# Kernel tuning notes

Measured on AMD Instinct MI355X. Metric: run time of the kernel, lower is better.

The kernel has to match this reference:

```python
import jax, jax.numpy as jnp
import numpy as np
from jax import lax

N, L, C_IN, NOISE_C, COMP, NC = 256, 512, 514, 112, 16, 2
MAIN_IN = NOISE_C + COMP  # 128
FEAT = NC * 4 * L         # 4096

def _conv1d(x, w, b, pad):
    # x [N,C,L], w [O,I,K]
    y = lax.conv_general_dilated(x, w, (1,), [(pad, pad)], dimension_numbers=('NCH', 'OIH', 'NCH'))
    return y + b[None, :, None]

def _bn(x, g, b):
    # BatchNorm1d, training mode: biased batch stats over (N, L)
    m = x.mean(axis=(0, 2), keepdims=True)
    v = x.var(axis=(0, 2), keepdims=True)
    return (x - m) * lax.rsqrt(v + 1e-5) * g[None, :, None] + b[None, :, None]

def _lrelu(x):
    return jnp.where(x >= 0, x, 0.2 * x)

def _pos_encode(length, dim):
    j = np.arange(dim)
    div = 1.0 / np.power(10000.0, 2 * (j[:, None] // 2) / dim)   # [dim,1]
    ang = np.arange(length)[None, :] * div                       # [dim,length]
    ang = np.where((j % 2 == 0)[:, None], np.sin(ang), np.cos(ang))
    return jnp.asarray(ang[None], jnp.float32)                   # [1,dim,length]

def _assemble(circle_prob, slider_prob):
    # Vectorized run-length label expansion equivalent to the per-sample python while-loop.
    # circle_prob [N, L/2, 2], slider_prob [N, L/4, 2] -> [N, L, 3]
    n, B = slider_prob.shape[0], slider_prob.shape[1]
    c = jnp.argmax(circle_prob, -1)
    s = jnp.argmax(slider_prob, -1)
    zc = jnp.zeros(circle_prob.shape[:-1] + (1,), circle_prob.dtype)
    zs = jnp.zeros(slider_prob.shape[:-1] + (1,), slider_prob.dtype)
    cp3 = jnp.concatenate([circle_prob, zc], -1)                                   # insert 0 at class 2
    sp3 = jnp.concatenate([slider_prob[..., :1], zs, slider_prob[..., 1:]], -1)    # insert 0 at class 1
    pad100 = jnp.array([1., 0., 0.], cp3.dtype)
    pad001 = jnp.array([0., 0., 1.], cp3.dtype)
    bidx = jnp.arange(B)[None, :]
    # slider-body blocks: slider run continues and not cut by sequence end
    body = (s == 1) & (bidx < B - 1)
    prev_body = jnp.concatenate([jnp.zeros((n, 1), bool), body[:, :-1]], 1)
    # tail block ends a slider run (either run stops, or boundary block)
    tail = ((s == 1) & (bidx == B - 1)) | ((s == 0) & prev_body)
    # circle emission for each half-step: prob row if predicted circle else pad
    cr0 = jnp.where((c == 1)[..., None], cp3, pad100).reshape(n, B, 2, 3)
    bodyE = body[..., None]
    row0 = jnp.where((body | tail)[..., None], sp3, cr0[:, :, 0, :])
    row1 = jnp.where(bodyE, pad001, pad100)
    row2 = jnp.where(bodyE, pad001, cr0[:, :, 1, :])
    row3 = jnp.where(bodyE, pad001, pad100)
    return jnp.stack([row0, row1, row2, row3], 2).reshape(n, 4 * B, 3)

def _forward(noise, cond_data, gumbel_u, ext_w1, ext_b1, ext_w2, ext_b2, ext_bn_g, ext_bn_b,
             m_w1, m_b1, m_w2, m_b2, m_bn_g, m_bn_b, lin_w, lin_b, circ_w, circ_b, slid_w, slid_b):
    # FeatureExtractor
    x = cond_data.transpose(0, 2, 1)                      # [N, 514, L]
    x = _lrelu(_conv1d(x, ext_w1, ext_b1, 0))             # [N, 32, L]
    cond = _bn(_conv1d(x, ext_w2, ext_b2, 1), ext_bn_g, ext_bn_b)  # [N, 16, L]
    gen_in = jnp.concatenate([cond, noise.transpose(0, 2, 1)], 1) + _pos_encode(L, MAIN_IN)  # [N,128,L]
    h = _lrelu(_conv1d(gen_in, m_w1, m_b1, 3))            # [N, 32, L]
    h = _lrelu(_bn(_conv1d(h, m_w2, m_b2, 1), m_bn_g, m_bn_b))     # [N, 8, L]
    flat = _lrelu(h.reshape(h.shape[0], -1) @ lin_w + lin_b)       # [N, 4096]
    circle_prob = (flat @ circ_w + circ_b).reshape(-1, L // 2, NC)
    slider_prob = (flat @ slid_w + slid_b).reshape(-1, L // 4, NC)
    out = _assemble(circle_prob, slider_prob)             # [N, L, 3]
    # gumbel_softmax(hard=True, tau=1)
    g = -jnp.log(-jnp.log(gumbel_u + 1e-10) + 1e-10)
    logits = out + g
    y_soft = jax.nn.softmax(logits, -1)
    y_hard = jax.nn.one_hot(jnp.argmax(logits, -1), 3, dtype=y_soft.dtype)
    gen_out = y_hard + y_soft - lax.stop_gradient(y_soft)
    return gen_out, cond

def setup_inputs() -> dict:
    key = jax.random.key(0)
    ks = jax.random.split(key, 12)
    def rn(k, shape, fan_in):
        return jax.random.normal(k, shape, jnp.float32) * (1.0 / fan_in) ** 0.5
    return {
        'noise': jax.random.normal(ks[0], (N, L, NOISE_C), jnp.float32),
        'cond_data': jax.random.normal(ks[1], (N, L, C_IN), jnp.float32),
        'gumbel_u': jax.random.uniform(ks[2], (N, L, 3), jnp.float32),
        'ext_w1': rn(ks[3], (C_IN // 16, C_IN, 1), C_IN), 'ext_b1': jnp.zeros(C_IN // 16),
        'ext_w2': rn(ks[4], (COMP, C_IN // 16, 3), 3 * (C_IN // 16)), 'ext_b2': jnp.zeros(COMP),
        'ext_bn_g': jnp.ones(COMP), 'ext_bn_b': jnp.zeros(COMP),
        'm_w1': rn(ks[5], (NC * 16, MAIN_IN, 7), 7 * MAIN_IN), 'm_b1': jnp.zeros(NC * 16),
        'm_w2': rn(ks[6], (NC * 4, NC * 16, 3), 3 * NC * 16), 'm_b2': jnp.zeros(NC * 4),
        'm_bn_g': jnp.ones(NC * 4), 'm_bn_b': jnp.zeros(NC * 4),
        'lin_w': rn(ks[7], (FEAT, FEAT), FEAT), 'lin_b': jnp.zeros(FEAT),
        'circ_w': rn(ks[8], (FEAT, NC * L // 2), FEAT), 'circ_b': jnp.zeros(NC * L // 2),
        'slid_w': rn(ks[9], (FEAT, NC * L // 4), FEAT), 'slid_b': jnp.zeros(NC * L // 4),
    }

def reference(noise, cond_data, gumbel_u, ext_w1, ext_b1, ext_w2, ext_b2, ext_bn_g, ext_bn_b,
              m_w1, m_b1, m_w2, m_b2, m_bn_g, m_bn_b, lin_w, lin_b, circ_w, circ_b, slid_w, slid_b):
    return _forward(noise, cond_data, gumbel_u, ext_w1, ext_b1, ext_w2, ext_b2, ext_bn_g, ext_bn_b,
                    m_w1, m_b1, m_w2, m_b2, m_bn_g, m_bn_b, lin_w, lin_b, circ_w, circ_b, slid_w, slid_b)
```

## Files before the change

### kernel.cpp

```cpp
#include <hip/hip_runtime.h>
#include <math.h>

#define NB 256
#define LL 512
#define CIN 514

__device__ __forceinline__ float lrelu(float x) { return x >= 0.f ? x : 0.2f * x; }

__global__ __launch_bounds__(256) void k_pos(float* __restrict__ pos) {
    int idx = blockIdx.x * 256 + threadIdx.x;
    int c = idx >> 9, l = idx & 511;
    double e = (double)(2 * (c >> 1)) / 128.0;
    double dv = 1.0 / pow(10000.0, e);
    double a = (double)l * dv;
    pos[idx] = (float)((c & 1) ? cos(a) : sin(a));
}

__global__ __launch_bounds__(256) void k_posconv(const float* __restrict__ POS, const float* __restrict__ W,
                                                 const float* __restrict__ bias, float* __restrict__ PC) {
    const int t = threadIdx.x;
    const int o = blockIdx.x >> 4, l0 = (blockIdx.x & 15) * 32;
    const int l = l0 + (t & 31), cs = t >> 5;
    float acc = 0.f;
    for (int ci = 0; ci < 16; ++ci) {
        int c = cs * 16 + ci;
        float wv[7];
#pragma unroll
        for (int k = 0; k < 7; ++k) wv[k] = W[o * 896 + c * 7 + k];
#pragma unroll
        for (int k = 0; k < 7; ++k) {
            int gl = l + k - 3;
            if (gl >= 0 && gl < LL) acc += wv[k] * POS[c * LL + gl];
        }
    }
    __shared__ float red[8][33];
    red[cs][t & 31] = acc;
    __syncthreads();
    if (cs == 0) {
        float s = bias[o];
#pragma unroll
        for (int j = 0; j < 8; ++j) s += red[j][t & 31];
        PC[o * LL + l0 + (t & 31)] = s;
    }
}

__global__ __launch_bounds__(256) void k_conv1(const float* __restrict__ X, const float* __restrict__ W,
                                               float* __restrict__ P0, float* __restrict__ P1) {
    __shared__ __align__(16) float As[16][524];
    __shared__ __align__(16) float Bs[16][36];
    const int t = threadIdx.x;
    const int n = blockIdx.x >> 1, z = blockIdx.x & 1;
    const int kbase = z * 256;
    const int nch = z ? 17 : 16;
    const int tl = t & 63, to = t >> 6;
    const size_t rowbase = (size_t)n * 512 * CIN;

    float acc[8][8];
#pragma unroll
    for (int oi = 0; oi < 8; ++oi)
#pragma unroll
        for (int p = 0; p < 8; ++p) acc[oi][p] = 0.f;

    float2 pf[16];
    float2 pfb;

    {
        const int kb = kbase;
#pragma unroll
        for (int ps = 0; ps < 16; ++ps) {
            int idx = ps * 256 + t;
            int pos = idx >> 3, kp = idx & 7;
            int gk = kb + kp * 2;
            float2 v = {0.f, 0.f};
            if (gk + 1 < CIN) v = *(const float2*)(X + rowbase + (size_t)pos * CIN + gk);
            else if (gk < CIN) v.x = X[rowbase + (size_t)pos * CIN + gk];
            pf[ps] = v;
        }
        {
            int o = t >> 3, kp = t & 7;
            int gk = kb + kp * 2;
            float2 v = {0.f, 0.f};
            if (gk + 1 < CIN) v = *(const float2*)(W + (size_t)o * CIN + gk);
            else if (gk < CIN) v.x = W[(size_t)o * CIN + gk];
            pfb = v;
        }
#pragma unroll
        for (int ps = 0; ps < 16; ++ps) {
            int idx = ps * 256 + t;
            int pos = idx >> 3, kp = idx & 7;
            As[kp * 2][pos] = pf[ps].x;
            As[kp * 2 + 1][pos] = pf[ps].y;
        }
        {
            int o = t >> 3, kp = t & 7;
            Bs[kp * 2][o] = pfb.x;
            Bs[kp * 2 + 1][o] = pfb.y;
        }
    }
    __syncthreads();

    for (int c = 0; c < nch; ++c) {
        if (c + 1 < nch) {
            const int kb = kbase + (c + 1) * 16;
#pragma unroll
            for (int ps = 0; ps < 16; ++ps) {
                int idx = ps * 256 + t;
                int pos = idx >> 3, kp = idx & 7;
                int gk = kb + kp * 2;
                float2 v = {0.f, 0.f};
                if (gk + 1 < CIN) v = *(const float2*)(X + rowbase + (size_t)pos * CIN + gk);
                else if (gk < CIN) v.x = X[rowbase + (size_t)pos * CIN + gk];
                pf[ps] = v;
            }
            int o = t >> 3, kp = t & 7;
            int gk = kb + kp * 2;
            float2 v = {0.f, 0.f};
            if (gk + 1 < CIN) v = *(const float2*)(W + (size_t)o * CIN + gk);
            else if (gk < CIN) v.x = W[(size_t)o * CIN + gk];
            pfb = v;
        }
#pragma unroll
        for (int kk = 0; kk < 16; ++kk) {
            float4 aL = *(const float4*)&As[kk][tl * 4];
            float4 aH = *(const float4*)&As[kk][256 + tl * 4];
            float4 b0 = *(const float4*)&Bs[kk][to * 8];
            float4 b1 = *(const float4*)&Bs[kk][to * 8 + 4];
            float av[8] = {aL.x, aL.y, aL.z, aL.w, aH.x, aH.y, aH.z, aH.w};
            float bv[8] = {b0.x, b0.y, b0.z, b0.w, b1.x, b1.y, b1.z, b1.w};
#pragma unroll
            for (int oi = 0; oi < 8; ++oi)
#pragma unroll
                for (int p = 0; p < 8; ++p) acc[oi][p] += av[p] * bv[oi];
        }
        __syncthreads();
        if (c + 1 < nch) {
#pragma unroll
            for (int ps = 0; ps < 16; ++ps) {
                int idx = ps * 256 + t;
                int pos = idx >> 3, kp = idx & 7;
                As[kp * 2][pos] = pf[ps].x;
                As[kp * 2 + 1][pos] = pf[ps].y;
            }
            int o = t >> 3, kp = t & 7;
            Bs[kp * 2][o] = pfb.x;
            Bs[kp * 2 + 1][o] = pfb.y;
        }
        __syncthreads();
    }

    float* P = z ? P1 : P0;
#pragma unroll
    for (int oi = 0; oi < 8; ++oi) {
        int o = to * 8 + oi;
        float4 v0 = {acc[oi][0], acc[oi][1], acc[oi][2], acc[oi][3]};
        float4 v1 = {acc[oi][4], acc[oi][5], acc[oi][6], acc[oi][7]};
        *(float4*)(P + ((size_t)n * 32 + o) * LL + tl * 4) = v0;
        *(float4*)(P + ((size_t)n * 32 + o) * LL + 256 + tl * 4) = v1;
    }
}

__global__ __launch_bounds__(256) void k_conv2(const float* __restrict__ P0, const float* __restrict__ P1,
                                               const float* __restrict__ b1, const float* __restrict__ W,
                                               const float* __restrict__ bias, float* __restrict__ out) {
    __shared__ __align__(16) float Xs[32][264];
    __shared__ __align__(16) float Ws[16][32][4];
    const int t = threadIdx.x;
    const int n = blockIdx.x >> 1, l0 = (blockIdx.x & 1) * 256;
    for (int idx = t; idx < 32 * 258; idx += 256) {
        int i = idx / 258, j = idx % 258;
        int gl = l0 - 1 + j;
        float v = 0.f;
        if (gl >= 0 && gl < LL) {
            size_t off = ((size_t)n * 32 + i) * LL + gl;
            v = lrelu(P0[off] + P1[off] + b1[i]);
        }
        Xs[i][j] = v;
    }
    for (int idx = t; idx < 1536; idx += 256) {
        int o = idx / 96, r = idx % 96;
        Ws[o][r / 3][r % 3] = W[idx];
    }
    __syncthreads();
    const int tx = t & 31, ty = t >> 5;
    float acc[2][8];
#pragma unroll
    for (int q = 0; q < 2; ++q)
#pragma unroll
        for (int p = 0; p < 8; ++p) acc[q][p] = 0.f;
    for (int i = 0; i < 32; ++i) {
        float4 a0 = *(const float4*)&Xs[i][tx*8];
        float4 a1 = *(const float4*)&Xs[i][tx*8+4];
        float4 a2 = *(const float4*)&Xs[i][tx*8+8];
        float a[12] = {a0.x,a0.y,a0.z,a0.w,a1.x,a1.y,a1.z,a1.w,a2.x,a2.y,a2.z,a2.w};
#pragma unroll
        for (int q = 0; q < 2; ++q) {
            float4 b = *(const float4*)&Ws[ty*2+q][i][0];
#pragma unroll
            for (int p = 0; p < 8; ++p)
                acc[q][p] += a[p]*b.x + a[p+1]*b.y + a[p+2]*b.z;
        }
    }
#pragma unroll
    for (int q = 0; q < 2; ++q) {
        int o = ty*2+q; float bb = bias[o];
#pragma unroll
        for (int h = 0; h < 2; ++h) {
            float4 v;
            v.x = acc[q][h*4+0] + bb; v.y = acc[q][h*4+1] + bb;
            v.z = acc[q][h*4+2] + bb; v.w = acc[q][h*4+3] + bb;
            *(float4*)(out + ((size_t)n*16 + o)*LL + l0 + tx*8 + h*4) = v;
        }
    }
}

__global__ __launch_bounds__(256) void k_redstats(const float* __restrict__ src, int C, float* __restrict__ part) {
    const int ch = blockIdx.x, sl = blockIdx.y, t = threadIdx.x;
    float s = 0.f, q = 0.f;
    for (int i = t; i < 4096; i += 256) {
        int n = sl*8 + (i >> 9), l = i & 511;
        float v = src[((size_t)n*C + ch)*LL + l];
        s += v; q += v*v;
    }
    __shared__ float rs[256], rq[256];
    rs[t] = s; rq[t] = q;
    __syncthreads();
    for (int off = 128; off > 0; off >>= 1) {
        if (t < off) { rs[t] += rs[t+off]; rq[t] += rq[t+off]; }
        __syncthreads();
    }
    if (t == 0) { part[(ch*32+sl)*2] = rs[0]; part[(ch*32+sl)*2+1] = rq[0]; }
}

__global__ void k_bnfinal(const float* __restrict__ part, const float* __restrict__ g,
                          const float* __restrict__ b, int C, float* __restrict__ ss) {
    int ch = threadIdx.x;
    if (ch >= C) return;
    float s = 0.f, q = 0.f;
    for (int j = 0; j < 32; ++j) { s += part[(ch*32 + j)*2]; q += part[(ch*32 + j)*2 + 1]; }
    float mean = s * (1.f/131072.f);
    float var = q * (1.f/131072.f) - mean*mean;
    float sc = g[ch] / sqrtf(var + 1e-5f);
    ss[ch] = sc;
    ss[C + ch] = b[ch] - mean * sc;
}

__global__ __launch_bounds__(256) void k_bnapply(const float* __restrict__ src, const float* __restrict__ ss,
        int C, float* __restrict__ dst, int act, int total4) {
    int i4 = blockIdx.x * 256 + threadIdx.x;
    if (i4 >= total4) return;
    int i = i4 << 2;
    int ch = (i >> 9) % C;
    float sc = ss[ch], sh = ss[C + ch];
    float4 v = reinterpret_cast<const float4*>(src)[i4];
    v.x = v.x*sc + sh; v.y = v.y*sc + sh; v.z = v.z*sc + sh; v.w = v.w*sc + sh;
    if (act) { v.x = lrelu(v.x); v.y = lrelu(v.y); v.z = lrelu(v.z); v.w = lrelu(v.w); }
    reinterpret_cast<float4*>(dst)[i4] = v;
}

__global__ __launch_bounds__(256) void k_mconv1(const float* __restrict__ C16, const float* __restrict__ NZ,
        const float* __restrict__ PC, const float* __restrict__ W,
        float* __restrict__ out0, float* __restrict__ out1) {
    __shared__ __align__(16) float Gs[16][264];
    __shared__ __align__(16) float Ws[32][16][8];
    const int t = threadIdx.x;
    const int n = blockIdx.x >> 2, l0 = ((blockIdx.x >> 1) & 1) * 256, z = blockIdx.x & 1;
    const int tx = t & 31, ty = t >> 5;
    float acc[4][8];
#pragma unroll
    for (int q = 0; q < 4; ++q)
#pragma unroll
        for (int p = 0; p < 8; ++p) acc[q][p] = 0.f;

    for (int cc = 0; cc < 4; ++cc) {
        const int ctg = z * 4 + cc;
        if (cc) __syncthreads();
        if (ctg == 0) {
            for (int idx = t; idx < 16*262; idx += 256) {
                int c = idx / 262, j = idx - c * 262;
                int gl = l0 - 3 + j;
                float v = 0.f;
                if (gl >= 0 && gl < LL) v = C16[((size_t)n*16 + c)*LL + gl];
                Gs[c][j] = v;
            }
        } else {
            int nc0 = ctg * 16 - 16;
            for (int idx = t; idx < 16*262; idx += 256) {
                int c = idx & 15, j = idx >> 4;
                int gl = l0 - 3 + j;
                float v = 0.f;
                if (gl >= 0 && gl < LL) v = NZ[((size_t)n*LL + gl)*112 + nc0 + c];
                Gs[c][j] = v;
            }
        }
        for (int idx = t; idx < 32*112; idx += 256) {
            int o = idx / 112, r = idx % 112;
            Ws[o][r / 7][r % 7] = W[(size_t)o*896 + ctg*112 + r];
        }
        __syncthreads();
        for (int ci = 0; ci < 16; ++ci) {
            float4 a0 = *(const float4*)&Gs[ci][tx*4];
            float4 a1 = *(const float4*)&Gs[ci][tx*4+4];
            float4 a2 = *(const float4*)&Gs[ci][tx*4+8];
            float4 a3 = *(const float4*)&Gs[ci][128+tx*4];
            float4 a4 = *(const float4*)&Gs[ci][128+tx*4+4];
            float4 a5 = *(const float4*)&Gs[ci][128+tx*4+8];
            float aA[12] = {a0.x,a0.y,a0.z,a0.w,a1.x,a1.y,a1.z,a1.w,a2.x,a2.y,a2.z,a2.w};
            float aB[12] = {a3.x,a3.y,a3.z,a3.w,a4.x,a4.y,a4.z,a4.w,a5.x,a5.y,a5.z,a5.w};
#pragma unroll
            for (int q = 0; q < 4; ++q) {
                float4 b0 = *(const float4*)&Ws[ty*4+q][ci][0];
                float4 b1 = *(const float4*)&Ws[ty*4+q][ci][4];
                float b[7] = {b0.x,b0.y,b0.z,b0.w,b1.x,b1.y,b1.z};
#pragma unroll
                for (int p = 0; p < 4; ++p) {
#pragma unroll
                    for (int k = 0; k < 7; ++k) {
                        acc[q][p]   += aA[p+k]*b[k];
                        acc[q][4+p] += aB[p+k]*b[k];
                    }
                }
            }
        }
    }
    float* out = z ? out1 : out0;
#pragma unroll
    for (int q = 0; q < 4; ++q) {
        int o = ty*4 + q;
        float4 p0 = {0.f,0.f,0.f,0.f}, p1 = {0.f,0.f,0.f,0.f};
        if (z == 0) {
            p0 = *(const float4*)(PC + o*LL + l0 + tx*4);
            p1 = *(const float4*)(PC + o*LL + l0 + 128 + tx*4);
        }
        float4 v0 = {acc[q][0]+p0.x, acc[q][1]+p0.y, acc[q][2]+p0.z, acc[q][3]+p0.w};
        float4 v1 = {acc[q][4]+p1.x, acc[q][5]+p1.y, acc[q][6]+p1.z, acc[q][7]+p1.w};
        *(float4*)(out + ((size_t)n*32 + o)*LL + l0 + tx*4) = v0;
        *(float4*)(out + ((size_t)n*32 + o)*LL + l0 + 128 + tx*4) = v1;
    }
}

__global__ __launch_bounds__(256) void k_mconv2(const float* __restrict__ P0, const float* __restrict__ P1,
        const float* __restrict__ W, const float* __restrict__ bias, float* __restrict__ out) {
    __shared__ __align__(16) float Xs[32][264];
    __shared__ __align__(16) float Ws[8][32][4];
    const int t = threadIdx.x;
    const int n = blockIdx.x >> 1, l0 = (blockIdx.x & 1) * 256;
    for (int idx = t; idx < 32 * 258; idx += 256) {
        int i = idx / 258, j = idx % 258;
        int gl = l0 - 1 + j;
        float v = 0.f;
        if (gl >= 0 && gl < LL) {
            size_t off = ((size_t)n * 32 + i) * LL + gl;
            v = lrelu(P0[off] + P1[off]);
        }
        Xs[i][j] = v;
    }
    for (int idx = t; idx < 768; idx += 256) {
        int o = idx / 96, r = idx % 96;
        Ws[o][r / 3][r % 3] = W[idx];
    }
    __syncthreads();
    const int tx = t & 31, ty = t >> 5;
    float acc[8];
#pragma unroll
    for (int p = 0; p < 8; ++p) acc[p] = 0.f;
    for (int i = 0; i < 32; ++i) {
        float4 a0 = *(const float4*)&Xs[i][tx*8];
        float4 a1 = *(const float4*)&Xs[i][tx*8+4];
        float4 a2 = *(const float4*)&Xs[i][tx*8+8];
        float a[12] = {a0.x,a0.y,a0.z,a0.w,a1.x,a1.y,a1.z,a1.w,a2.x,a2.y,a2.z,a2.w};
        float4 b = *(const float4*)&Ws[ty][i][0];
#pragma unroll
        for (int p = 0; p < 8; ++p)
            acc[p] += a[p]*b.x + a[p+1]*b.y + a[p+2]*b.z;
    }
    float bb = bias[ty];
#pragma unroll
    for (int h = 0; h < 2; ++h) {
        float4 v;
        v.x = acc[h*4+0] + bb; v.y = acc[h*4+1] + bb;
        v.z = acc[h*4+2] + bb; v.w = acc[h*4+3] + bb;
        *(float4*)(out + ((size_t)n*8 + ty)*LL + l0 + tx*8 + h*4) = v;
    }
}

__global__ __launch_bounds__(256) void k_lin(const float* __restrict__ A, const float* __restrict__ B,
                                             float* __restrict__ part) {
    __shared__ __align__(16) float As[32][68];
    __shared__ __align__(16) float Bs[32][68];
    const int t = threadIdx.x;
    const int bid = blockIdx.x;
    const int x = bid & 7, j = bid >> 3;
    const int f0 = (x * 8 + (j & 7)) * 64;
    const int m0 = ((j >> 3) & 3) * 64;
    const int z = j >> 5;
    const int lane = t & 63, wv = t >> 6;
    const int smi = t & 63, skq = t >> 6;
    const int ski = t >> 3, sf4 = t & 7;
    const int k0base = z * 2048;

    const int ar = wv * 16 + ((lane >> 4) << 2);
    const int br = (lane & 15) << 2;

    float acc[4][4];
#pragma unroll
    for (int i = 0; i < 4; ++i)
#pragma unroll
        for (int q = 0; q < 4; ++q) acc[i][q] = 0.f;

    float4 pa0, pa1, pb0, pb1;
    {
        const float* pA = A + (size_t)(m0 + smi) * 4096 + k0base;
        pa0 = *(const float4*)(pA + skq * 4);
        pa1 = *(const float4*)(pA + skq * 4 + 16);
        const float* pB = B + (size_t)(k0base + ski) * 4096 + f0;
        pb0 = *(const float4*)(pB + sf4 * 4);
        pb1 = *(const float4*)(pB + sf4 * 4 + 32);
        As[skq*4+0][smi] = pa0.x; As[skq*4+1][smi] = pa0.y; As[skq*4+2][smi] = pa0.z; As[skq*4+3][smi] = pa0.w;
        As[skq*4+16][smi] = pa1.x; As[skq*4+17][smi] = pa1.y; As[skq*4+18][smi] = pa1.z; As[skq*4+19][smi] = pa1.w;
        *(float4*)&Bs[ski][sf4*4] = pb0;
        *(float4*)&Bs[ski][sf4*4+32] = pb1;
    }
    __syncthreads();

    for (int it = 0; it < 64; ++it) {
        if (it + 1 < 64) {
            const int k0 = k0base + (it + 1) * 32;
            const float* pA = A + (size_t)(m0 + smi) * 4096 + k0;
            pa0 = *(const float4*)(pA + skq * 4);
            pa1 = *(const float4*)(pA + skq * 4 + 16);
            const float* pB = B + (size_t)(k0 + ski) * 4096 + f0;
            pb0 = *(const float4*)(pB + sf4 * 4);
            pb1 = *(const float4*)(pB + sf4 * 4 + 32);
        }
#pragma unroll
        for (int kk = 0; kk < 32; ++kk) {
            float4 a = *(const float4*)&As[kk][ar];
            float4 b = *(const float4*)&Bs[kk][br];
            float av[4] = {a.x, a.y, a.z, a.w};
            float bv[4] = {b.x, b.y, b.z, b.w};
#pragma unroll
            for (int i = 0; i < 4; ++i)
#pragma unroll
                for (int q = 0; q < 4; ++q) acc[i][q] += av[i] * bv[q];
        }
        __syncthreads();
        if (it + 1 < 64) {
            As[skq*4+0][smi] = pa0.x; As[skq*4+1][smi] = pa0.y; As[skq*4+2][smi] = pa0.z; As[skq*4+3][smi] = pa0.w;
            As[skq*4+16][smi] = pa1.x; As[skq*4+17][smi] = pa1.y; As[skq*4+18][smi] = pa1.z; As[skq*4+19][smi] = pa1.w;
            *(float4*)&Bs[ski][sf4*4] = pb0;
            *(float4*)&Bs[ski][sf4*4+32] = pb1;
        }
        __syncthreads();
    }

#pragma unroll
    for (int i = 0; i < 4; ++i) {
        int m = m0 + ar + i;
        float4 v = {acc[i][0], acc[i][1], acc[i][2], acc[i][3]};
        *(float4*)(part + ((size_t)z * 256 + m) * 4096 + f0 + br) = v;
    }
}

__global__ __launch_bounds__(256) void k_linred(const float* __restrict__ part, const float* __restrict__ bias,
        float* __restrict__ out) {
    int i4 = blockIdx.x*256 + threadIdx.x;
    int i = i4 << 2;
    int f = i & 4095;
    float4 a = ((const float4*)part)[i4];
    float4 c = ((const float4*)(part + 1048576))[i4];
    float4 bb = *(const float4*)(bias + f);
    float4 r;
    r.x = lrelu(a.x + c.x + bb.x);
    r.y = lrelu(a.y + c.y + bb.y);
    r.z = lrelu(a.z + c.z + bb.z);
    r.w = lrelu(a.w + c.w + bb.w);
    ((float4*)out)[i4] = r;
}

__global__ __launch_bounds__(256) void k_heads(const float* __restrict__ A, const float* __restrict__ CW,
        const float* __restrict__ SW, float* __restrict__ part) {
    __shared__ __align__(16) float As[32][36];
    __shared__ __align__(16) float Bs[32][132];
    const int t = threadIdx.x;
    const int m0 = blockIdx.x * 32, f0 = blockIdx.y * 128, z = blockIdx.z;
    const float* B; int ldb, fb;
    if (f0 < 512) { B = CW; ldb = 512; fb = f0; } else { B = SW; ldb = 256; fb = f0 - 512; }
    const int tm = t & 7, tf = t >> 3;
    const int mi = t >> 3, kq = t & 7;
    float acc[4][4];
#pragma unroll
    for (int pm = 0; pm < 4; ++pm)
#pragma unroll
        for (int pf = 0; pf < 4; ++pf) acc[pm][pf] = 0.f;
    for (int k0 = z * 512; k0 < z * 512 + 512; k0 += 32) {
        float4 av = *(const float4*)(A + (size_t)(m0 + mi) * 4096 + k0 + kq * 4);
        As[kq*4+0][mi] = av.x; As[kq*4+1][mi] = av.y; As[kq*4+2][mi] = av.z; As[kq*4+3][mi] = av.w;
#pragma unroll
        for (int pass = 0; pass < 4; ++pass) {
            int fi = pass * 32 + kq * 4;
            *(float4*)&Bs[mi][fi] = *(const float4*)(B + (size_t)(k0 + mi) * ldb + fb + fi);
        }
        __syncthreads();
#pragma unroll 8
        for (int kk = 0; kk < 32; ++kk) {
            float4 a = *(const float4*)&As[kk][tm * 4];
            float4 b = *(const float4*)&Bs[kk][tf * 4];
            float avv[4] = {a.x,a.y,a.z,a.w};
            float bvv[4] = {b.x,b.y,b.z,b.w};
#pragma unroll
            for (int pm = 0; pm < 4; ++pm)
#pragma unroll
                for (int pf = 0; pf < 4; ++pf) acc[pm][pf] += avv[pm]*bvv[pf];
        }
        __syncthreads();
    }
#pragma unroll
    for (int pm = 0; pm < 4; ++pm) {
        float4 v = {acc[pm][0], acc[pm][1], acc[pm][2], acc[pm][3]};
        *(float4*)(part + ((size_t)z * 256 + m0 + tm * 4 + pm) * 768 + f0 + tf * 4) = v;
    }
}

__global__ __launch_bounds__(256) void k_headred(const float* __restrict__ part, const float* __restrict__ cb,
        const float* __restrict__ sb, float* __restrict__ circ, float* __restrict__ slid) {
    int i4 = blockIdx.x * 256 + threadIdx.x;
    int i = i4 << 2;
    int n = i / 768, f = i % 768;
    float4 s = {0.f,0.f,0.f,0.f};
#pragma unroll
    for (int ks = 0; ks < 8; ++ks) {
        float4 p = *(const float4*)(part + ((size_t)ks*256 + n)*768 + f);
        s.x += p.x; s.y += p.y; s.z += p.z; s.w += p.w;
    }
    if (f < 512) {
        float4 bb = *(const float4*)(cb + f);
        s.x += bb.x; s.y += bb.y; s.z += bb.z; s.w += bb.w;
        *(float4*)(circ + (size_t)n*512 + f) = s;
    } else {
        float4 bb = *(const float4*)(sb + f - 512);
        s.x += bb.x; s.y += bb.y; s.z += bb.z; s.w += bb.w;
        *(float4*)(slid + (size_t)n*256 + f - 512) = s;
    }
}

__global__ __launch_bounds__(128) void k_assemble(const float* __restrict__ circ, const float* __restrict__ slid,
        const float* __restrict__ gum, float* __restrict__ out) {
    const int n = blockIdx.x;
    const int b = threadIdx.x;
    const float* sp = slid + (size_t)n * 256;
    const float* cp = circ + (size_t)n * 512;
    float sl0 = sp[2*b], sl1 = sp[2*b+1];
    int s = sl1 > sl0 ? 1 : 0;
    int prevb = 0;
    if (b > 0) prevb = (sp[2*b-1] > sp[2*b-2]) ? 1 : 0;
    bool body = (s == 1) && (b < 127);
    bool tail = ((s == 1) && (b == 127)) || ((s == 0) && (prevb == 1));
    float c0a = cp[4*b], c0b = cp[4*b+1], c1a = cp[4*b+2], c1b = cp[4*b+3];
    bool cA = c0b > c0a, cB = c1b > c1a;
    float rows[4][3];
    if (body || tail)      { rows[0][0]=sl0; rows[0][1]=0.f; rows[0][2]=sl1; }
    else if (cA)           { rows[0][0]=c0a; rows[0][1]=c0b; rows[0][2]=0.f; }
    else                   { rows[0][0]=1.f; rows[0][1]=0.f; rows[0][2]=0.f; }
    if (body)              { rows[1][0]=0.f; rows[1][1]=0.f; rows[1][2]=1.f; }
    else                   { rows[1][0]=1.f; rows[1][1]=0.f; rows[1][2]=0.f; }
    if (body)              { rows[2][0]=0.f; rows[2][1]=0.f; rows[2][2]=1.f; }
    else if (cB)           { rows[2][0]=c1a; rows[2][1]=c1b; rows[2][2]=0.f; }
    else                   { rows[2][0]=1.f; rows[2][1]=0.f; rows[2][2]=0.f; }
    rows[3][0]=rows[1][0]; rows[3][1]=rows[1][1]; rows[3][2]=rows[1][2];
#pragma unroll
    for (int r = 0; r < 4; ++r) {
        int l = 4*b + r;
        const float* u = gum + ((size_t)n*512 + l)*3;
        float g0 = -logf(-logf(u[0]+1e-10f)+1e-10f);
        float g1 = -logf(-logf(u[1]+1e-10f)+1e-10f);
        float g2 = -logf(-logf(u[2]+1e-10f)+1e-10f);
        float t0 = rows[r][0]+g0, t1 = rows[r][1]+g1, t2 = rows[r][2]+g2;
        int am = 0; float mv = t0;
        if (t1 > mv) { am = 1; mv = t1; }
        if (t2 > mv) { am = 2; mv = t2; }
        float e0 = expf(t0-mv), e1 = expf(t1-mv), e2 = expf(t2-mv);
        float ssum = e0+e1+e2;
        float y0 = e0/ssum, y1 = e1/ssum, y2 = e2/ssum;
        float* o = out + ((size_t)n*512 + l)*3;
        o[0] = ((am==0?1.f:0.f) + y0) - y0;
        o[1] = ((am==1?1.f:0.f) + y1) - y1;
        o[2] = ((am==2?1.f:0.f) + y2) - y2;
    }
}

extern "C" void kernel_launch(void* const* d_in, const int* in_sizes, int n_in,
                              void* d_out, int out_size, void* d_ws, size_t ws_size,
                              hipStream_t stream) {
    const float* noise   = (const float*)d_in[0];
    const float* cond    = (const float*)d_in[1];
    const float* gumbel  = (const float*)d_in[2];
    const float* ext_w1  = (const float*)d_in[3];
    const float* ext_b1  = (const float*)d_in[4];
    const float* ext_w2  = (const float*)d_in[5];
    const float* ext_b2  = (const float*)d_in[6];
    const float* ext_bng = (const float*)d_in[7];
    const float* ext_bnb = (const float*)d_in[8];
    const float* m_w1    = (const float*)d_in[9];
    const float* m_b1    = (const float*)d_in[10];
    const float* m_w2    = (const float*)d_in[11];
    const float* m_b2    = (const float*)d_in[12];
    const float* m_bng   = (const float*)d_in[13];
    const float* m_bnb   = (const float*)d_in[14];
    const float* lin_w   = (const float*)d_in[15];
    const float* lin_b   = (const float*)d_in[16];
    const float* circ_w  = (const float*)d_in[17];
    const float* circ_b  = (const float*)d_in[18];
    const float* slid_w  = (const float*)d_in[19];
    const float* slid_b  = (const float*)d_in[20];

    float* genout  = (float*)d_out;
    float* condout = (float*)d_out + 256*512*3;

    float* w     = (float*)d_ws;
    float* x1    = w;
    float* y2    = x1 + 4194304;
    float* posb  = y2 + 2097152;
    float* circ  = posb + 65536;
    float* slid  = circ + 131072;
    float* flatB = slid + 65536;
    float* partL = flatB + 1048576;
    float* partH = partL + 2097152;
    float* stats = partH + 1572864;
    float* pc    = stats + 4096;
    float* buf1  = flatB;

    k_pos<<<256, 256, 0, stream>>>(posb);
    k_posconv<<<512, 256, 0, stream>>>(posb, m_w1, m_b1, pc);
    k_conv1<<<512, 256, 0, stream>>>(cond, ext_w1, x1, buf1);
    k_conv2<<<512, 256, 0, stream>>>(x1, buf1, ext_b1, ext_w2, ext_b2, y2);
    k_redstats<<<dim3(16,32), 256, 0, stream>>>(y2, 16, stats);
    k_bnfinal<<<1, 64, 0, stream>>>(stats, ext_bng, ext_bnb, 16, stats + 2048);
    k_bnapply<<<2048, 256, 0, stream>>>(y2, stats + 2048, 16, condout, 0, 524288);
    k_mconv1<<<1024, 256, 0, stream>>>(condout, noise, pc, m_w1, x1, buf1);
    k_mconv2<<<512, 256, 0, stream>>>(x1, buf1, m_w2, m_b2, y2);
    k_redstats<<<dim3(8,32), 256, 0, stream>>>(y2, 8, stats);
    k_bnfinal<<<1, 64, 0, stream>>>(stats, m_bng, m_bnb, 8, stats + 2048 + 64);
    k_bnapply<<<1024, 256, 0, stream>>>(y2, stats + 2048 + 64, 8, y2, 1, 262144);
    k_lin<<<512, 256, 0, stream>>>(y2, lin_w, partL);
    k_linred<<<1024, 256, 0, stream>>>(partL, lin_b, flatB);
    k_heads<<<dim3(8,6,8), 256, 0, stream>>>(flatB, circ_w, slid_w, partH);
    k_headred<<<192, 256, 0, stream>>>(partH, circ_b, slid_b, circ, slid);
    k_assemble<<<256, 128, 0, stream>>>(circ, slid, gumbel, genout);
}
```

Before: 579.6 us.

## Split linear GEMM K four ways with XCD-aware block mapping, drop register prefetch

The large 256x4096x4096 linear GEMM now splits K into four chunks instead of two, which doubles the grid to 1024 blocks. The block-index mapping is reordered so that blocks on the same XCD share an f0 column tile, aiming for better L2 reuse of the weight tile. The register-prefetch double-buffering is removed in favour of a simpler load-sync-compute loop. The reduction kernel now sums four partials, and the partials buffer moves to x1, which must be large enough to hold them. This trades more partial-sum traffic and less latency hiding for higher occupancy and locality.

```diff
diff --git a/kernel.cpp b/kernel.cpp
--- a/kernel.cpp
+++ b/kernel.cpp
@@ -389,14 +389,15 @@
     __shared__ __align__(16) float Bs[32][68];
     const int t = threadIdx.x;
     const int bid = blockIdx.x;
-    const int x = bid & 7, j = bid >> 3;
-    const int f0 = (x * 8 + (j & 7)) * 64;
-    const int m0 = ((j >> 3) & 3) * 64;
-    const int z = j >> 5;
+    const int xcd = bid & 7, idx = bid >> 3;
+    const int f0 = (xcd * 8 + (idx >> 4)) * 64;
+    const int sub = idx & 15;
+    const int m0 = (sub & 3) * 64;
+    const int z = sub >> 2;
     const int lane = t & 63, wv = t >> 6;
     const int smi = t & 63, skq = t >> 6;
     const int ski = t >> 3, sf4 = t & 7;
-    const int k0base = z * 2048;
+    const int k0base = z * 1024;
 
     const int ar = wv * 16 + ((lane >> 4) << 2);
     const int br = (lane & 15) << 2;
@@ -407,31 +408,21 @@
 #pragma unroll
         for (int q = 0; q < 4; ++q) acc[i][q] = 0.f;
 
-    float4 pa0, pa1, pb0, pb1;
-    {
-        const float* pA = A + (size_t)(m0 + smi) * 4096 + k0base;
-        pa0 = *(const float4*)(pA + skq * 4);
-        pa1 = *(const float4*)(pA + skq * 4 + 16);
-        const float* pB = B + (size_t)(k0base + ski) * 4096 + f0;
-        pb0 = *(const float4*)(pB + sf4 * 4);
-        pb1 = *(const float4*)(pB + sf4 * 4 + 32);
-        As[skq*4+0][smi] = pa0.x; As[skq*4+1][smi] = pa0.y; As[skq*4+2][smi] = pa0.z; As[skq*4+3][smi] = pa0.w;
-        As[skq*4+16][smi] = pa1.x; As[skq*4+17][smi] = pa1.y; As[skq*4+18][smi] = pa1.z; As[skq*4+19][smi] = pa1.w;
-        *(float4*)&Bs[ski][sf4*4] = pb0;
-        *(float4*)&Bs[ski][sf4*4+32] = pb1;
-    }
-    __syncthreads();
-
-    for (int it = 0; it < 64; ++it) {
-        if (it + 1 < 64) {
-            const int k0 = k0base + (it + 1) * 32;
+    for (int it = 0; it < 32; ++it) {
+        const int k0 = k0base + it * 32;
+        {
             const float* pA = A + (size_t)(m0 + smi) * 4096 + k0;
-            pa0 = *(const float4*)(pA + skq * 4);
-            pa1 = *(const float4*)(pA + skq * 4 + 16);
+            float4 a0 = *(const float4*)(pA + skq * 4);
+            float4 a1 = *(const float4*)(pA + skq * 4 + 16);
             const float* pB = B + (size_t)(k0 + ski) * 4096 + f0;
-            pb0 = *(const float4*)(pB + sf4 * 4);
-            pb1 = *(const float4*)(pB + sf4 * 4 + 32);
-        }
+            float4 b0 = *(const float4*)(pB + sf4 * 4);
+            float4 b1 = *(const float4*)(pB + sf4 * 4 + 32);
+            As[skq*4+0][smi] = a0.x; As[skq*4+1][smi] = a0.y; As[skq*4+2][smi] = a0.z; As[skq*4+3][smi] = a0.w;
+            As[skq*4+16][smi] = a1.x; As[skq*4+17][smi] = a1.y; As[skq*4+18][smi] = a1.z; As[skq*4+19][smi] = a1.w;
+            *(float4*)&Bs[ski][sf4*4] = b0;
+            *(float4*)&Bs[ski][sf4*4+32] = b1;
+        }
+        __syncthreads();
 #pragma unroll
         for (int kk = 0; kk < 32; ++kk) {
             float4 a = *(const float4*)&As[kk][ar];
@@ -442,13 +433,6 @@
             for (int i = 0; i < 4; ++i)
 #pragma unroll
                 for (int q = 0; q < 4; ++q) acc[i][q] += av[i] * bv[q];
-        }
-        __syncthreads();
-        if (it + 1 < 64) {
-            As[skq*4+0][smi] = pa0.x; As[skq*4+1][smi] = pa0.y; As[skq*4+2][smi] = pa0.z; As[skq*4+3][smi] = pa0.w;
-            As[skq*4+16][smi] = pa1.x; As[skq*4+17][smi] = pa1.y; As[skq*4+18][smi] = pa1.z; As[skq*4+19][smi] = pa1.w;
-            *(float4*)&Bs[ski][sf4*4] = pb0;
-            *(float4*)&Bs[ski][sf4*4+32] = pb1;
         }
         __syncthreads();
     }
@@ -467,13 +451,15 @@
     int i = i4 << 2;
     int f = i & 4095;
     float4 a = ((const float4*)part)[i4];
-    float4 c = ((const float4*)(part + 1048576))[i4];
+    float4 b = ((const float4*)(part + 1048576))[i4];
+    float4 c = ((const float4*)(part + 2097152))[i4];
+    float4 d = ((const float4*)(part + 3145728))[i4];
     float4 bb = *(const float4*)(bias + f);
     float4 r;
-    r.x = lrelu(a.x + c.x + bb.x);
-    r.y = lrelu(a.y + c.y + bb.y);
-    r.z = lrelu(a.z + c.z + bb.z);
-    r.w = lrelu(a.w + c.w + bb.w);
+    r.x = lrelu(a.x + b.x + c.x + d.x + bb.x);
+    r.y = lrelu(a.y + b.y + c.y + d.y + bb.y);
+    r.z = lrelu(a.z + b.z + c.z + d.z + bb.z);
+    r.w = lrelu(a.w + b.w + c.w + d.w + bb.w);
     ((float4*)out)[i4] = r;
 }
 
@@ -641,8 +627,8 @@
     k_redstats<<<dim3(8,32), 256, 0, stream>>>(y2, 8, stats);
     k_bnfinal<<<1, 64, 0, stream>>>(stats, m_bng, m_bnb, 8, stats + 2048 + 64);
     k_bnapply<<<1024, 256, 0, stream>>>(y2, stats + 2048 + 64, 8, y2, 1, 262144);
-    k_lin<<<512, 256, 0, stream>>>(y2, lin_w, partL);
-    k_linred<<<1024, 256, 0, stream>>>(partL, lin_b, flatB);
+    k_lin<<<1024, 256, 0, stream>>>(y2, lin_w, x1);
+    k_linred<<<1024, 256, 0, stream>>>(x1, lin_b, flatB);
     k_heads<<<dim3(8,6,8), 256, 0, stream>>>(flatB, circ_w, slid_w, partH);
     k_headred<<<192, 256, 0, stream>>>(partH, circ_b, slid_b, circ, slid);
     k_assemble<<<256, 128, 0, stream>>>(circ, slid, gumbel, genout);
```

New measurement: 554.7 us. 4.3% less time.
